# Kernel optimization log

Hardware: AMD Instinct MI355X
Metric: run time of the kernel (lower is better)

## Reference

```python
import jax, jax.numpy as jnp
import numpy as np

B_, L_, D_, E_, N_, DT_, K_ = 2, 1024, 1024, 2048, 16, 64, 4
EPS = 1e-5


def setup_inputs() -> dict:
    key = jax.random.key(0)
    ks = jax.random.split(key, 16)
    s = lambda *sh: 1.0 / np.sqrt(sh[-1])
    return {
        "resid": jax.random.normal(ks[0], (B_, L_, D_), jnp.float32),
        "norm_w": jnp.ones((D_,), jnp.float32),
        "skip_w": jax.random.normal(ks[1], (E_, D_), jnp.float32) * s(E_, D_),
        "in_w": jax.random.normal(ks[2], (E_, D_), jnp.float32) * s(E_, D_),
        "conv_w": jax.random.normal(ks[3], (E_, K_), jnp.float32) * s(E_, K_),
        "conv_b": jax.random.normal(ks[4], (E_,), jnp.float32) * 0.1,
        "wd1": jax.random.normal(ks[5], (DT_, E_), jnp.float32) * s(DT_, E_),
        "wd2": jax.random.normal(ks[6], (E_, DT_), jnp.float32) * s(E_, DT_),
        "wd2_b": jax.random.normal(ks[7], (E_,), jnp.float32) * 0.1,
        "wb": jax.random.normal(ks[8], (N_, E_), jnp.float32) * s(N_, E_),
        "wc": jax.random.normal(ks[9], (N_, E_), jnp.float32) * s(N_, E_),
        "A_log": jnp.log(jax.random.uniform(ks[10], (E_, N_), jnp.float32, 0.5, 4.0)),
        "W_D": jnp.ones((E_,), jnp.float32),
        "out_w": jax.random.normal(ks[11], (D_, E_), jnp.float32) * s(D_, E_),
    }


def _forward(resid, norm_w, skip_w, in_w, conv_w, conv_b, wd1, wd2, wd2_b,
             wb, wc, A_log, W_D, out_w):
    B, L, D = resid.shape
    E, N = A_log.shape
    K = conv_w.shape[-1]
    # RMSNorm
    xn = resid * jax.lax.rsqrt(jnp.mean(resid * resid, -1, keepdims=True) + EPS) * norm_w
    skip = jnp.einsum('bld,ed->ble', xn, skip_w)
    x = jnp.einsum('bld,ed->ble', xn, in_w)
    # causal depthwise conv1d (torch pads both sides by K-1, output cut to [:L])
    xp = jnp.pad(x, ((0, 0), (K - 1, 0), (0, 0)))
    conv = conv_b + sum(xp[:, k:k + L, :] * conv_w[:, k] for k in range(K))
    x = jax.nn.silu(conv)  # [B,L,E] ssm input
    # input-dependent projections
    delta = jax.nn.softplus(jnp.einsum('ble,re->blr', x, wd1) @ wd2.T + wd2_b)  # [B,L,E]
    Bt = jnp.einsum('ble,ne->bln', x, wb)  # [B,L,N]
    Ct = jnp.einsum('ble,ne->bln', x, wc)  # [B,L,N]
    A = -jnp.exp(A_log)  # [E,N]

    def step(h, inp):
        dt, b_t, c_t, x_t = inp  # [B,E],[B,N],[B,N],[B,E]
        A_bar = jnp.exp(dt[:, :, None] * A)          # [B,E,N]
        h = A_bar * h + (dt * x_t)[:, :, None] * b_t[:, None, :]
        y = jnp.einsum('ben,bn->be', h, c_t)
        return h, y

    h0 = jnp.zeros((B, E, N), x.dtype)
    xs = (delta.transpose(1, 0, 2), Bt.transpose(1, 0, 2),
          Ct.transpose(1, 0, 2), x.transpose(1, 0, 2))
    _, y = jax.lax.scan(step, h0, xs)
    y = y.transpose(1, 0, 2)  # [B,L,E]
    y = y + x * W_D
    y = y * jax.nn.silu(skip)
    y = jnp.einsum('ble,de->bld', y, out_w)
    return resid + y


def reference(resid, norm_w, skip_w, in_w, conv_w, conv_b, wd1, wd2, wd2_b,
              wb, wc, A_log, W_D, out_w):
    return _forward(resid, norm_w, skip_w, in_w, conv_w, conv_b, wd1, wd2,
                    wd2_b, wb, wc, A_log, W_D, out_w)
```

## Files before the change

kernel.cpp:

```cpp
#include <hip/hip_runtime.h>
#include <cstdint>

typedef unsigned short u16;
typedef float f32x4 __attribute__((ext_vector_type(4)));
typedef __bf16 bf16x8 __attribute__((ext_vector_type(8)));
typedef u16 u16x8 __attribute__((ext_vector_type(8)));

__device__ __forceinline__ u16 f2bf(float f) {
  uint32_t u = __float_as_uint(f);
  u += 0x7fffu + ((u >> 16) & 1u);
  return (u16)(u >> 16);
}
__device__ __forceinline__ float bf2f(u16 s) {
  return __uint_as_float(((uint32_t)s) << 16);
}

__device__ __forceinline__ void ld16(const u16* g, u16* l) {
  auto* gp = reinterpret_cast<const __attribute__((address_space(1))) u16*>(
      reinterpret_cast<uintptr_t>(g));
  auto* lp = reinterpret_cast<__attribute__((address_space(3))) u16*>(
      static_cast<uint32_t>(reinterpret_cast<uintptr_t>(l)));
  __builtin_amdgcn_global_load_lds(gp, lp, 16, 0, 0);
}

__device__ __forceinline__ f32x4 mfma16(u16x8 a, u16x8 b, f32x4 c) {
  return __builtin_amdgcn_mfma_f32_16x16x32_bf16(
      __builtin_bit_cast(bf16x8, a), __builtin_bit_cast(bf16x8, b), c, 0, 0, 0);
}

__device__ __forceinline__ float sigmoidf_(float x) { return 1.f / (1.f + __expf(-x)); }
__device__ __forceinline__ float siluf_(float x) { return x * sigmoidf_(x); }
__device__ __forceinline__ float softplusf_(float x) {
  return fmaxf(x, 0.f) + log1pf(__expf(-fabsf(x)));
}

#define PACK_TOT 6651904
__global__ __launch_bounds__(256) void pack_rms_kernel(
    const float* __restrict__ skip_w, const float* __restrict__ in_w,
    const float* __restrict__ out_w, const float* __restrict__ wd2,
    const float* __restrict__ wd1, const float* __restrict__ wb,
    const float* __restrict__ wc, const float* __restrict__ A_log,
    u16* __restrict__ skipw_bf, u16* __restrict__ inw_bf, u16* __restrict__ outw_bf,
    u16* __restrict__ wd2_bf, u16* __restrict__ w96, float* __restrict__ Aneg,
    const float* __restrict__ resid, const float* __restrict__ norm_w,
    u16* __restrict__ xn_bf) {
  int t = threadIdx.x;
  if (blockIdx.x >= 1024) {
    int row = blockIdx.x - 1024;
    const float4* xr = (const float4*)(resid + (size_t)row * 1024);
    float4 v = xr[t];
    float ss = v.x * v.x + v.y * v.y + v.z * v.z + v.w * v.w;
    for (int o = 32; o > 0; o >>= 1) ss += __shfl_xor(ss, o);
    __shared__ float wsum[4];
    if ((t & 63) == 0) wsum[t >> 6] = ss;
    __syncthreads();
    float tot = wsum[0] + wsum[1] + wsum[2] + wsum[3];
    float rs = rsqrtf(tot * (1.0f / 1024.0f) + 1e-5f);
    float4 wv = ((const float4*)norm_w)[t];
    uint2 pk;
    pk.x = (uint32_t)f2bf(v.x * rs * wv.x) | ((uint32_t)f2bf(v.y * rs * wv.y) << 16);
    pk.y = (uint32_t)f2bf(v.z * rs * wv.z) | ((uint32_t)f2bf(v.w * rs * wv.w) << 16);
    ((uint2*)xn_bf)[row * 256 + t] = pk;
    return;
  }
  const int stride = 1024 * 256;
  for (int i = blockIdx.x * 256 + t; i < PACK_TOT; i += stride) {
    int j = i;
    if (j < 2097152) { skipw_bf[j] = f2bf(skip_w[j]); continue; } j -= 2097152;
    if (j < 2097152) { inw_bf[j] = f2bf(in_w[j]); continue; } j -= 2097152;
    if (j < 2097152) { outw_bf[j] = f2bf(out_w[j]); continue; } j -= 2097152;
    if (j < 131072)  { wd2_bf[j] = f2bf(wd2[j]); continue; } j -= 131072;
    if (j < 131072)  { w96[j] = f2bf(wd1[j]); continue; } j -= 131072;
    if (j < 32768)   { w96[131072 + j] = f2bf(wb[j]); continue; } j -= 32768;
    if (j < 32768)   { w96[163840 + j] = f2bf(wc[j]); continue; } j -= 32768;
    Aneg[j] = -__expf(A_log[j]);
  }
}

template <int BM, int BN, int BK, int EPI>
__global__ __launch_bounds__(256) void gemm_bt(
    const u16* __restrict__ A, const u16* __restrict__ B0, const u16* __restrict__ B1,
    int M, int N, int K, int Nsplit,
    void* __restrict__ C0, void* __restrict__ C1,
    const float* __restrict__ bias, const float* __restrict__ addsrc) {
  constexpr int TM = BM / 32, TN = BN / 32;
  constexpr int KC = BK / 8;
  __shared__ __align__(16) u16 sA[BM * BK];
  __shared__ __align__(16) u16 sB[BN * BK];
  const int t = threadIdx.x;
  const int lane = t & 63, wid = t >> 6;
  const int wm = wid >> 1, wn = wid & 1;
  const int mBase = blockIdx.y * BM;
  const int nBase = blockIdx.x * BN;
  const bool hi = (nBase >= Nsplit);
  const u16* Bp = hi ? B1 : B0;
  const int nB0 = nBase - (hi ? Nsplit : 0);
  const int col = lane & 15, quad = lane >> 4;

  f32x4 acc[TM][TN];
#pragma unroll
  for (int i = 0; i < TM; ++i)
#pragma unroll
    for (int j = 0; j < TN; ++j) acc[i][j] = f32x4{0.f, 0.f, 0.f, 0.f};

  for (int k0 = 0; k0 < K; k0 += BK) {
#pragma unroll
    for (int c = t; c < BM * KC; c += 256) {
      int row = c / KC, j = c % KC;
      int k8 = ((j + row) & (KC - 1)) * 8;
      ld16(A + (size_t)(mBase + row) * K + k0 + k8, &sA[c * 8]);
    }
#pragma unroll
    for (int c = t; c < BN * KC; c += 256) {
      int row = c / KC, j = c % KC;
      int k8 = ((j + row) & (KC - 1)) * 8;
      ld16(Bp + (size_t)(nB0 + row) * K + k0 + k8, &sB[c * 8]);
    }
    __syncthreads();
#pragma unroll
    for (int kk = 0; kk < BK / 32; ++kk) {
      u16x8 af[TM], bfv[TN];
#pragma unroll
      for (int i = 0; i < TM; ++i) {
        int rowA = wm * (BM / 2) + i * 16 + col;
        af[i] = *(const u16x8*)&sA[rowA * BK + (((kk * 4 + quad) - rowA) & (KC - 1)) * 8];
      }
#pragma unroll
      for (int j = 0; j < TN; ++j) {
        int rowB = wn * (BN / 2) + j * 16 + col;
        bfv[j] = *(const u16x8*)&sB[rowB * BK + (((kk * 4 + quad) - rowB) & (KC - 1)) * 8];
      }
#pragma unroll
      for (int i = 0; i < TM; ++i)
#pragma unroll
        for (int j = 0; j < TN; ++j) acc[i][j] = mfma16(af[i], bfv[j], acc[i][j]);
    }
    __syncthreads();
  }

#pragma unroll
  for (int i = 0; i < TM; ++i) {
#pragma unroll
    for (int j = 0; j < TN; ++j) {
#pragma unroll
      for (int r = 0; r < 4; ++r) {
        int gm = mBase + wm * (BM / 2) + i * 16 + quad * 4 + r;
        int gn = nBase + wn * (BN / 2) + j * 16 + col;
        float v = acc[i][j][r];
        if (EPI == 0) {
          if (gn < Nsplit)
            ((u16*)C0)[(size_t)gm * Nsplit + gn] = f2bf(v);
          else
            ((u16*)C1)[(size_t)gm * (N - Nsplit) + (gn - Nsplit)] = f2bf(v);
        } else if (EPI == 1) {
          ((u16*)C0)[(size_t)gm * N + gn] = f2bf(softplusf_(v + bias[gn]));
        } else {
          ((float*)C0)[(size_t)gm * N + gn] = addsrc[(size_t)gm * N + gn] + v;
        }
      }
    }
  }
}

__global__ __launch_bounds__(256) void conv_skinny_kernel(
    const u16* __restrict__ xin_bf, const float* __restrict__ conv_w,
    const float* __restrict__ conv_b, u16* __restrict__ xconv_bf,
    const u16* __restrict__ w96, float* __restrict__ part) {
  constexpr int PAD = 264;
  __shared__ __align__(16) u16 sA[64 * PAD];
  __shared__ __align__(16) u16 sB[96 * 128];
  const int t = threadIdx.x, lane = t & 63, w = t >> 6;
  const int mBase = blockIdx.x * 64;
  const int e0 = blockIdx.y * 256;

  {
    const int ep = (t & 127) * 2;
    const int strip = t >> 7;
    const int ms = mBase + strip * 32;
    const int l0 = ms & 1023;
    const uint32_t* xr = (const uint32_t*)xin_bf;
    size_t base = ((size_t)ms * 2048 + e0 + ep) >> 1;
    int eg = e0 + ep;
    float4 w0 = ((const float4*)conv_w)[eg];
    float4 w1 = ((const float4*)conv_w)[eg + 1];
    float b0 = conv_b[eg], b1 = conv_b[eg + 1];
    uint32_t u;
    u = (l0 >= 1) ? xr[base - 1024] : 0u;
    float h10 = bf2f((u16)u), h11 = bf2f((u16)(u >> 16));
    u = (l0 >= 2) ? xr[base - 2048] : 0u;
    float h20 = bf2f((u16)u), h21 = bf2f((u16)(u >> 16));
    u = (l0 >= 3) ? xr[base - 3072] : 0u;
    float h30 = bf2f((u16)u), h31 = bf2f((u16)(u >> 16));
#pragma unroll 4
    for (int r = 0; r < 32; ++r) {
      uint32_t ux = xr[base + (size_t)r * 1024];
      float x0 = bf2f((u16)ux), x1 = bf2f((u16)(ux >> 16));
      float a0 = b0 + w0.w * x0 + w0.z * h10 + w0.y * h20 + w0.x * h30;
      float a1 = b1 + w1.w * x1 + w1.z * h11 + w1.y * h21 + w1.x * h31;
      a0 = siluf_(a0); a1 = siluf_(a1);
      uint32_t pk = (uint32_t)f2bf(a0) | ((uint32_t)f2bf(a1) << 16);
      ((uint32_t*)xconv_bf)[base + (size_t)r * 1024] = pk;
      *(uint32_t*)&sA[(strip * 32 + r) * PAD + ep] = pk;
      h30 = h20; h31 = h21; h20 = h10; h21 = h11; h10 = x0; h11 = x1;
    }
  }
  for (int c = t; c < 96 * 16; c += 256) {
    int row = c >> 4, j = c & 15;
    int k8 = ((j + row) & 15) * 8;
    ld16(w96 + (size_t)row * 2048 + e0 + k8, &sB[c * 8]);
  }
  __syncthreads();
  const int col = lane & 15, quad = lane >> 4;
  const int rowA = w * 16 + col;
  f32x4 acc[6];
#pragma unroll
  for (int j = 0; j < 6; ++j) acc[j] = f32x4{0.f, 0.f, 0.f, 0.f};
#pragma unroll
  for (int kk = 0; kk < 4; ++kk) {
    u16x8 af = *(const u16x8*)&sA[rowA * PAD + kk * 32 + quad * 8];
#pragma unroll
    for (int j = 0; j < 6; ++j) {
      int rowB = j * 16 + col;
      u16x8 bfv = *(const u16x8*)&sB[rowB * 128 + (((kk * 4 + quad) - rowB) & 15) * 8];
      acc[j] = mfma16(af, bfv, acc[j]);
    }
  }
  __syncthreads();
  for (int c = t; c < 96 * 16; c += 256) {
    int row = c >> 4, j = c & 15;
    int k8 = ((j + row) & 15) * 8;
    ld16(w96 + (size_t)row * 2048 + e0 + 128 + k8, &sB[c * 8]);
  }
  __syncthreads();
#pragma unroll
  for (int kk = 4; kk < 8; ++kk) {
    u16x8 af = *(const u16x8*)&sA[rowA * PAD + kk * 32 + quad * 8];
#pragma unroll
    for (int j = 0; j < 6; ++j) {
      int rowB = j * 16 + col;
      u16x8 bfv = *(const u16x8*)&sB[rowB * 128 + ((((kk - 4) * 4 + quad) - rowB) & 15) * 8];
      acc[j] = mfma16(af, bfv, acc[j]);
    }
  }
  float* pp = part + (size_t)blockIdx.y * (2048 * 96);
#pragma unroll
  for (int j = 0; j < 6; ++j)
#pragma unroll
    for (int r = 0; r < 4; ++r) {
      int gm = mBase + w * 16 + quad * 4 + r;
      int gn = j * 16 + col;
      pp[gm * 96 + gn] = acc[j][r];
    }
}

__global__ __launch_bounds__(256) void skinny_reduce(
    const float* __restrict__ part, u16* __restrict__ d1_bf,
    float* __restrict__ bc) {
  int i = blockIdx.x * 256 + threadIdx.x;
  float s = 0.f;
#pragma unroll
  for (int kc = 0; kc < 8; ++kc) s += part[kc * 196608 + i];
  int m = i / 96, n = i - m * 96;
  if (n < 64) d1_bf[m * 64 + n] = f2bf(s);
  else bc[m * 32 + n - 64] = s;
}

__global__ __launch_bounds__(256) void scan1_kernel(
    const u16* __restrict__ delta_bf, const u16* __restrict__ xconv_bf,
    const float* __restrict__ bc, const float* __restrict__ Aneg,
    float* __restrict__ hloc, float* __restrict__ Ssum) {
  int t = threadIdx.x;
  int e = blockIdx.x * 256 + t;
  int c = blockIdx.y, b = blockIdx.z;
  int m0 = b * 1024 + c * 32;
  __shared__ float sBC[1024];
  for (int j = t; j < 1024; j += 256) sBC[j] = bc[m0 * 32 + j];
  float Ar[16], h[16];
#pragma unroll
  for (int n = 0; n < 16; ++n) { Ar[n] = Aneg[e * 16 + n]; h[n] = 0.f; }
  float S = 0.f;
  __syncthreads();
  for (int l = 0; l < 32; ++l) {
    size_t m = (size_t)(m0 + l) * 2048 + e;
    float dt = bf2f(delta_bf[m]), xv = bf2f(xconv_bf[m]);
    S += dt;
    float dx = dt * xv;
    const float* bl = &sBC[l * 32];
#pragma unroll
    for (int n = 0; n < 16; ++n) h[n] = __expf(dt * Ar[n]) * h[n] + dx * bl[n];
  }
  size_t base = ((size_t)(b * 32 + c) * 2048 + e) * 16;
#pragma unroll
  for (int n = 0; n < 16; ++n) hloc[base + n] = h[n];
  Ssum[(b * 32 + c) * 2048 + e] = S;
}

__global__ __launch_bounds__(256) void combine_kernel(
    const float* __restrict__ Aneg, const float* __restrict__ Ssum,
    float* __restrict__ hloc) {
  int tid = blockIdx.x * 256 + threadIdx.x;
  int b = tid >> 15, r = tid & 32767;
  int e = r >> 4;
  float a = Aneg[r];
  float h = 0.f;
  for (int c = 0; c < 32; ++c) {
    size_t base = (size_t)(b * 32 + c) * 32768 + r;
    float hl = hloc[base];
    float S = Ssum[(b * 32 + c) * 2048 + e];
    hloc[base] = h;
    h = __expf(a * S) * h + hl;
  }
}

__global__ __launch_bounds__(256) void scan2_kernel(
    const u16* __restrict__ delta_bf, const u16* __restrict__ xconv_bf,
    const float* __restrict__ bc, const float* __restrict__ Aneg,
    const float* __restrict__ hloc, const u16* __restrict__ skip_bf,
    const float* __restrict__ W_D, u16* __restrict__ yfin_bf) {
  int t = threadIdx.x;
  int e = blockIdx.x * 256 + t;
  int c = blockIdx.y, b = blockIdx.z;
  int m0 = b * 1024 + c * 32;
  __shared__ float sBC[1024];
  for (int j = t; j < 1024; j += 256) sBC[j] = bc[m0 * 32 + j];
  float Ar[16], h[16];
  size_t hbase = ((size_t)(b * 32 + c) * 2048 + e) * 16;
#pragma unroll
  for (int n = 0; n < 16; ++n) { Ar[n] = Aneg[e * 16 + n]; h[n] = hloc[hbase + n]; }
  float wd = W_D[e];
  __syncthreads();
  for (int l = 0; l < 32; ++l) {
    size_t m = (size_t)(m0 + l) * 2048 + e;
    float dt = bf2f(delta_bf[m]), xv = bf2f(xconv_bf[m]);
    float dx = dt * xv;
    const float* bl = &sBC[l * 32];
    float y = 0.f;
#pragma unroll
    for (int n = 0; n < 16; ++n) {
      h[n] = __expf(dt * Ar[n]) * h[n] + dx * bl[n];
      y += h[n] * bl[16 + n];
    }
    float yv = y + xv * wd;
    float sk = bf2f(skip_bf[m]);
    yv *= sk * sigmoidf_(sk);
    yfin_bf[m] = f2bf(yv);
  }
}

extern "C" void kernel_launch(void* const* d_in, const int* in_sizes, int n_in,
                              void* d_out, int out_size, void* d_ws, size_t ws_size,
                              hipStream_t stream) {
  (void)in_sizes; (void)n_in; (void)out_size; (void)ws_size;
  const float* resid  = (const float*)d_in[0];
  const float* norm_w = (const float*)d_in[1];
  const float* skip_w = (const float*)d_in[2];
  const float* in_w   = (const float*)d_in[3];
  const float* conv_w = (const float*)d_in[4];
  const float* conv_b = (const float*)d_in[5];
  const float* wd1    = (const float*)d_in[6];
  const float* wd2    = (const float*)d_in[7];
  const float* wd2_b  = (const float*)d_in[8];
  const float* wb     = (const float*)d_in[9];
  const float* wc     = (const float*)d_in[10];
  const float* A_log  = (const float*)d_in[11];
  const float* W_D    = (const float*)d_in[12];
  const float* out_w  = (const float*)d_in[13];

  char* p = (char*)d_ws;
  u16*   skipw_bf = (u16*)(p + 0);
  u16*   inw_bf   = (u16*)(p + 4194304);
  u16*   outw_bf  = (u16*)(p + 8388608);
  u16*   wd2_bf   = (u16*)(p + 12582912);
  u16*   w96      = (u16*)(p + 12845056);
  float* Aneg     = (float*)(p + 13238272);
  u16*   xn_bf    = (u16*)(p + 13369344);
  u16*   skip_bf  = (u16*)(p + 17563648);
  u16*   xin_bf   = (u16*)(p + 25952256);
  u16*   xconv_bf = (u16*)(p + 34340864);
  u16*   delta_bf = (u16*)(p + 42729472);
  u16*   d1_bf    = (u16*)(p + 51118080);
  float* bc       = (float*)(p + 51380224);
  u16*   yfin_bf  = (u16*)(p + 51642368);
  float* part     = (float*)(p + 60030976);
  float* hloc     = (float*)(p + 66322432);
  float* Ssum     = (float*)(p + 74711040);

  pack_rms_kernel<<<3072, 256, 0, stream>>>(
      skip_w, in_w, out_w, wd2, wd1, wb, wc, A_log,
      skipw_bf, inw_bf, outw_bf, wd2_bf, w96, Aneg,
      resid, norm_w, xn_bf);
  gemm_bt<128, 128, 64, 0><<<dim3(32, 16), 256, 0, stream>>>(
      xn_bf, skipw_bf, inw_bf, 2048, 4096, 1024, 2048,
      (void*)skip_bf, (void*)xin_bf, nullptr, nullptr);
  conv_skinny_kernel<<<dim3(32, 8), 256, 0, stream>>>(
      xin_bf, conv_w, conv_b, xconv_bf, w96, part);
  skinny_reduce<<<768, 256, 0, stream>>>(part, d1_bf, bc);
  gemm_bt<128, 128, 64, 1><<<dim3(16, 16), 256, 0, stream>>>(
      d1_bf, wd2_bf, wd2_bf, 2048, 2048, 64, 2048,
      (void*)delta_bf, nullptr, wd2_b, nullptr);
  scan1_kernel<<<dim3(8, 32, 2), 256, 0, stream>>>(delta_bf, xconv_bf, bc, Aneg,
                                                   hloc, Ssum);
  combine_kernel<<<256, 256, 0, stream>>>(Aneg, Ssum, hloc);
  scan2_kernel<<<dim3(8, 32, 2), 256, 0, stream>>>(delta_bf, xconv_bf, bc, Aneg, hloc,
                                                   skip_bf, W_D, yfin_bf);
  gemm_bt<64, 64, 128, 2><<<dim3(16, 32), 256, 0, stream>>>(
      yfin_bf, outw_bf, outw_bf, 2048, 1024, 2048, 1024,
      (void*)d_out, nullptr, nullptr, resid);
}
```

Baseline: 232.5 us.

## Fuse all pipeline stages into one persistent kernel with grid barriers

```diff
diff --git a/kernel.cpp b/kernel.cpp
--- a/kernel.cpp
+++ b/kernel.cpp
@@ -5,6 +5,9 @@
 typedef float f32x4 __attribute__((ext_vector_type(4)));
 typedef __bf16 bf16x8 __attribute__((ext_vector_type(8)));
 typedef u16 u16x8 __attribute__((ext_vector_type(8)));
+
+#define NBLK 512
+#define PACK_TOT 6651904
 
 __device__ __forceinline__ u16 f2bf(float f) {
   uint32_t u = __float_as_uint(f);
@@ -34,64 +37,43 @@
   return fmaxf(x, 0.f) + log1pf(__expf(-fabsf(x)));
 }
 
-#define PACK_TOT 6651904
-__global__ __launch_bounds__(256) void pack_rms_kernel(
-    const float* __restrict__ skip_w, const float* __restrict__ in_w,
-    const float* __restrict__ out_w, const float* __restrict__ wd2,
-    const float* __restrict__ wd1, const float* __restrict__ wb,
-    const float* __restrict__ wc, const float* __restrict__ A_log,
-    u16* __restrict__ skipw_bf, u16* __restrict__ inw_bf, u16* __restrict__ outw_bf,
-    u16* __restrict__ wd2_bf, u16* __restrict__ w96, float* __restrict__ Aneg,
-    const float* __restrict__ resid, const float* __restrict__ norm_w,
-    u16* __restrict__ xn_bf) {
-  int t = threadIdx.x;
-  if (blockIdx.x >= 1024) {
-    int row = blockIdx.x - 1024;
-    const float4* xr = (const float4*)(resid + (size_t)row * 1024);
-    float4 v = xr[t];
-    float ss = v.x * v.x + v.y * v.y + v.z * v.z + v.w * v.w;
-    for (int o = 32; o > 0; o >>= 1) ss += __shfl_xor(ss, o);
-    __shared__ float wsum[4];
-    if ((t & 63) == 0) wsum[t >> 6] = ss;
-    __syncthreads();
-    float tot = wsum[0] + wsum[1] + wsum[2] + wsum[3];
-    float rs = rsqrtf(tot * (1.0f / 1024.0f) + 1e-5f);
-    float4 wv = ((const float4*)norm_w)[t];
-    uint2 pk;
-    pk.x = (uint32_t)f2bf(v.x * rs * wv.x) | ((uint32_t)f2bf(v.y * rs * wv.y) << 16);
-    pk.y = (uint32_t)f2bf(v.z * rs * wv.z) | ((uint32_t)f2bf(v.w * rs * wv.w) << 16);
-    ((uint2*)xn_bf)[row * 256 + t] = pk;
-    return;
-  }
-  const int stride = 1024 * 256;
-  for (int i = blockIdx.x * 256 + t; i < PACK_TOT; i += stride) {
-    int j = i;
-    if (j < 2097152) { skipw_bf[j] = f2bf(skip_w[j]); continue; } j -= 2097152;
-    if (j < 2097152) { inw_bf[j] = f2bf(in_w[j]); continue; } j -= 2097152;
-    if (j < 2097152) { outw_bf[j] = f2bf(out_w[j]); continue; } j -= 2097152;
-    if (j < 131072)  { wd2_bf[j] = f2bf(wd2[j]); continue; } j -= 131072;
-    if (j < 131072)  { w96[j] = f2bf(wd1[j]); continue; } j -= 131072;
-    if (j < 32768)   { w96[131072 + j] = f2bf(wb[j]); continue; } j -= 32768;
-    if (j < 32768)   { w96[163840 + j] = f2bf(wc[j]); continue; } j -= 32768;
-    Aneg[j] = -__expf(A_log[j]);
-  }
-}
+__device__ __forceinline__ void gsync(uint32_t* bar, int idx) {
+  __syncthreads();
+  if (threadIdx.x == 0) {
+    __threadfence();
+    __hip_atomic_fetch_add(&bar[idx], 1u, __ATOMIC_RELEASE, __HIP_MEMORY_SCOPE_AGENT);
+    while (__hip_atomic_load(&bar[idx], __ATOMIC_ACQUIRE,
+                             __HIP_MEMORY_SCOPE_AGENT) < (uint32_t)NBLK) {
+      __builtin_amdgcn_s_sleep(1);
+    }
+    __threadfence();
+  }
+  __syncthreads();
+}
+
+struct Args {
+  const float *resid, *norm_w, *skip_w, *in_w, *conv_w, *conv_b, *wd1, *wd2,
+      *wd2_b, *wb, *wc, *A_log, *W_D, *out_w;
+  u16 *skipw_bf, *inw_bf, *outw_bf, *wd2_bf, *w96, *xn_bf, *skip_bf, *xin_bf,
+      *xconv_bf, *delta_bf, *d1_bf, *yfin_bf;
+  float *Aneg, *bc, *part, *hloc, *Ssum, *out;
+  uint32_t* bar;
+};
 
 template <int BM, int BN, int BK, int EPI>
-__global__ __launch_bounds__(256) void gemm_bt(
-    const u16* __restrict__ A, const u16* __restrict__ B0, const u16* __restrict__ B1,
-    int M, int N, int K, int Nsplit,
+__device__ void gemm_phase(char* smem, int bx, int by,
+    const u16* __restrict__ A, const u16* __restrict__ B0,
+    const u16* __restrict__ B1, int N, int K, int Nsplit,
     void* __restrict__ C0, void* __restrict__ C1,
     const float* __restrict__ bias, const float* __restrict__ addsrc) {
-  constexpr int TM = BM / 32, TN = BN / 32;
-  constexpr int KC = BK / 8;
-  __shared__ __align__(16) u16 sA[BM * BK];
-  __shared__ __align__(16) u16 sB[BN * BK];
+  constexpr int TM = BM / 32, TN = BN / 32, KC = BK / 8;
+  u16* sA = (u16*)smem;
+  u16* sB = (u16*)smem + BM * BK;
   const int t = threadIdx.x;
   const int lane = t & 63, wid = t >> 6;
   const int wm = wid >> 1, wn = wid & 1;
-  const int mBase = blockIdx.y * BM;
-  const int nBase = blockIdx.x * BN;
+  const int mBase = by * BM;
+  const int nBase = bx * BN;
   const bool hi = (nBase >= Nsplit);
   const u16* Bp = hi ? B1 : B0;
   const int nB0 = nBase - (hi ? Nsplit : 0);
@@ -162,28 +144,25 @@
   }
 }
 
-__global__ __launch_bounds__(256) void conv_skinny_kernel(
-    const u16* __restrict__ xin_bf, const float* __restrict__ conv_w,
-    const float* __restrict__ conv_b, u16* __restrict__ xconv_bf,
-    const u16* __restrict__ w96, float* __restrict__ part) {
+__device__ void conv_skinny_phase(char* smem, int bxm, int byk, const Args& a) {
   constexpr int PAD = 264;
-  __shared__ __align__(16) u16 sA[64 * PAD];
-  __shared__ __align__(16) u16 sB[96 * 128];
+  u16* sA = (u16*)smem;
+  u16* sB = (u16*)(smem + 64 * PAD * 2);
   const int t = threadIdx.x, lane = t & 63, w = t >> 6;
-  const int mBase = blockIdx.x * 64;
-  const int e0 = blockIdx.y * 256;
+  const int mBase = bxm * 64;
+  const int e0 = byk * 256;
 
   {
     const int ep = (t & 127) * 2;
     const int strip = t >> 7;
     const int ms = mBase + strip * 32;
     const int l0 = ms & 1023;
-    const uint32_t* xr = (const uint32_t*)xin_bf;
+    const uint32_t* xr = (const uint32_t*)a.xin_bf;
     size_t base = ((size_t)ms * 2048 + e0 + ep) >> 1;
     int eg = e0 + ep;
-    float4 w0 = ((const float4*)conv_w)[eg];
-    float4 w1 = ((const float4*)conv_w)[eg + 1];
-    float b0 = conv_b[eg], b1 = conv_b[eg + 1];
+    float4 w0 = ((const float4*)a.conv_w)[eg];
+    float4 w1 = ((const float4*)a.conv_w)[eg + 1];
+    float b0 = a.conv_b[eg], b1 = a.conv_b[eg + 1];
     uint32_t u;
     u = (l0 >= 1) ? xr[base - 1024] : 0u;
     float h10 = bf2f((u16)u), h11 = bf2f((u16)(u >> 16));
@@ -199,7 +178,7 @@
       float a1 = b1 + w1.w * x1 + w1.z * h11 + w1.y * h21 + w1.x * h31;
       a0 = siluf_(a0); a1 = siluf_(a1);
       uint32_t pk = (uint32_t)f2bf(a0) | ((uint32_t)f2bf(a1) << 16);
-      ((uint32_t*)xconv_bf)[base + (size_t)r * 1024] = pk;
+      ((uint32_t*)a.xconv_bf)[base + (size_t)r * 1024] = pk;
       *(uint32_t*)&sA[(strip * 32 + r) * PAD + ep] = pk;
       h30 = h20; h31 = h21; h20 = h10; h21 = h11; h10 = x0; h11 = x1;
     }
@@ -207,7 +186,7 @@
   for (int c = t; c < 96 * 16; c += 256) {
     int row = c >> 4, j = c & 15;
     int k8 = ((j + row) & 15) * 8;
-    ld16(w96 + (size_t)row * 2048 + e0 + k8, &sB[c * 8]);
+    ld16(a.w96 + (size_t)row * 2048 + e0 + k8, &sB[c * 8]);
   }
   __syncthreads();
   const int col = lane & 15, quad = lane >> 4;
@@ -229,7 +208,7 @@
   for (int c = t; c < 96 * 16; c += 256) {
     int row = c >> 4, j = c & 15;
     int k8 = ((j + row) & 15) * 8;
-    ld16(w96 + (size_t)row * 2048 + e0 + 128 + k8, &sB[c * 8]);
+    ld16(a.w96 + (size_t)row * 2048 + e0 + 128 + k8, &sB[c * 8]);
   }
   __syncthreads();
 #pragma unroll
@@ -242,7 +221,7 @@
       acc[j] = mfma16(af, bfv, acc[j]);
     }
   }
-  float* pp = part + (size_t)blockIdx.y * (2048 * 96);
+  float* pp = a.part + (size_t)byk * (2048 * 96);
 #pragma unroll
   for (int j = 0; j < 6; ++j)
 #pragma unroll
@@ -253,97 +232,153 @@
     }
 }
 
-__global__ __launch_bounds__(256) void skinny_reduce(
-    const float* __restrict__ part, u16* __restrict__ d1_bf,
-    float* __restrict__ bc) {
-  int i = blockIdx.x * 256 + threadIdx.x;
-  float s = 0.f;
-#pragma unroll
-  for (int kc = 0; kc < 8; ++kc) s += part[kc * 196608 + i];
-  int m = i / 96, n = i - m * 96;
-  if (n < 64) d1_bf[m * 64 + n] = f2bf(s);
-  else bc[m * 32 + n - 64] = s;
-}
-
-__global__ __launch_bounds__(256) void scan1_kernel(
-    const u16* __restrict__ delta_bf, const u16* __restrict__ xconv_bf,
-    const float* __restrict__ bc, const float* __restrict__ Aneg,
-    float* __restrict__ hloc, float* __restrict__ Ssum) {
-  int t = threadIdx.x;
-  int e = blockIdx.x * 256 + t;
-  int c = blockIdx.y, b = blockIdx.z;
-  int m0 = b * 1024 + c * 32;
-  __shared__ float sBC[1024];
-  for (int j = t; j < 1024; j += 256) sBC[j] = bc[m0 * 32 + j];
-  float Ar[16], h[16];
-#pragma unroll
-  for (int n = 0; n < 16; ++n) { Ar[n] = Aneg[e * 16 + n]; h[n] = 0.f; }
-  float S = 0.f;
-  __syncthreads();
-  for (int l = 0; l < 32; ++l) {
-    size_t m = (size_t)(m0 + l) * 2048 + e;
-    float dt = bf2f(delta_bf[m]), xv = bf2f(xconv_bf[m]);
-    S += dt;
-    float dx = dt * xv;
-    const float* bl = &sBC[l * 32];
-#pragma unroll
-    for (int n = 0; n < 16; ++n) h[n] = __expf(dt * Ar[n]) * h[n] + dx * bl[n];
-  }
-  size_t base = ((size_t)(b * 32 + c) * 2048 + e) * 16;
-#pragma unroll
-  for (int n = 0; n < 16; ++n) hloc[base + n] = h[n];
-  Ssum[(b * 32 + c) * 2048 + e] = S;
-}
-
-__global__ __launch_bounds__(256) void combine_kernel(
-    const float* __restrict__ Aneg, const float* __restrict__ Ssum,
-    float* __restrict__ hloc) {
-  int tid = blockIdx.x * 256 + threadIdx.x;
-  int b = tid >> 15, r = tid & 32767;
-  int e = r >> 4;
-  float a = Aneg[r];
-  float h = 0.f;
-  for (int c = 0; c < 32; ++c) {
-    size_t base = (size_t)(b * 32 + c) * 32768 + r;
-    float hl = hloc[base];
-    float S = Ssum[(b * 32 + c) * 2048 + e];
-    hloc[base] = h;
-    h = __expf(a * S) * h + hl;
-  }
-}
-
-__global__ __launch_bounds__(256) void scan2_kernel(
-    const u16* __restrict__ delta_bf, const u16* __restrict__ xconv_bf,
-    const float* __restrict__ bc, const float* __restrict__ Aneg,
-    const float* __restrict__ hloc, const u16* __restrict__ skip_bf,
-    const float* __restrict__ W_D, u16* __restrict__ yfin_bf) {
-  int t = threadIdx.x;
-  int e = blockIdx.x * 256 + t;
-  int c = blockIdx.y, b = blockIdx.z;
-  int m0 = b * 1024 + c * 32;
-  __shared__ float sBC[1024];
-  for (int j = t; j < 1024; j += 256) sBC[j] = bc[m0 * 32 + j];
-  float Ar[16], h[16];
-  size_t hbase = ((size_t)(b * 32 + c) * 2048 + e) * 16;
-#pragma unroll
-  for (int n = 0; n < 16; ++n) { Ar[n] = Aneg[e * 16 + n]; h[n] = hloc[hbase + n]; }
-  float wd = W_D[e];
-  __syncthreads();
-  for (int l = 0; l < 32; ++l) {
-    size_t m = (size_t)(m0 + l) * 2048 + e;
-    float dt = bf2f(delta_bf[m]), xv = bf2f(xconv_bf[m]);
-    float dx = dt * xv;
-    const float* bl = &sBC[l * 32];
-    float y = 0.f;
-#pragma unroll
-    for (int n = 0; n < 16; ++n) {
-      h[n] = __expf(dt * Ar[n]) * h[n] + dx * bl[n];
-      y += h[n] * bl[16 + n];
-    }
-    float yv = y + xv * wd;
-    float sk = bf2f(skip_bf[m]);
-    yv *= sk * sigmoidf_(sk);
-    yfin_bf[m] = f2bf(yv);
+__global__ __launch_bounds__(256, 2) void mega_kernel(Args a) {
+  __shared__ __align__(16) char smem[58368];
+  const int bid = blockIdx.x;
+  const int t = threadIdx.x;
+
+  for (int v = bid; v < 3072; v += NBLK) {
+    if (v >= 1024) {
+      int row = v - 1024;
+      const float4* xr = (const float4*)(a.resid + (size_t)row * 1024);
+      float4 vv = xr[t];
+      float ss = vv.x * vv.x + vv.y * vv.y + vv.z * vv.z + vv.w * vv.w;
+      for (int o = 32; o > 0; o >>= 1) ss += __shfl_xor(ss, o);
+      float* wsum = (float*)smem;
+      if ((t & 63) == 0) wsum[t >> 6] = ss;
+      __syncthreads();
+      float tot = wsum[0] + wsum[1] + wsum[2] + wsum[3];
+      float rs = rsqrtf(tot * (1.0f / 1024.0f) + 1e-5f);
+      float4 wv = ((const float4*)a.norm_w)[t];
+      uint2 pk;
+      pk.x = (uint32_t)f2bf(vv.x * rs * wv.x) | ((uint32_t)f2bf(vv.y * rs * wv.y) << 16);
+      pk.y = (uint32_t)f2bf(vv.z * rs * wv.z) | ((uint32_t)f2bf(vv.w * rs * wv.w) << 16);
+      ((uint2*)a.xn_bf)[row * 256 + t] = pk;
+      __syncthreads();
+    } else {
+      for (int i = v * 256 + t; i < PACK_TOT; i += 1024 * 256) {
+        int j = i;
+        if (j < 2097152) { a.skipw_bf[j] = f2bf(a.skip_w[j]); continue; } j -= 2097152;
+        if (j < 2097152) { a.inw_bf[j] = f2bf(a.in_w[j]); continue; } j -= 2097152;
+        if (j < 2097152) { a.outw_bf[j] = f2bf(a.out_w[j]); continue; } j -= 2097152;
+        if (j < 131072)  { a.wd2_bf[j] = f2bf(a.wd2[j]); continue; } j -= 131072;
+        if (j < 131072)  { a.w96[j] = f2bf(a.wd1[j]); continue; } j -= 131072;
+        if (j < 32768)   { a.w96[131072 + j] = f2bf(a.wb[j]); continue; } j -= 32768;
+        if (j < 32768)   { a.w96[163840 + j] = f2bf(a.wc[j]); continue; } j -= 32768;
+        a.Aneg[j] = -__expf(a.A_log[j]);
+      }
+    }
+  }
+  gsync(a.bar, 0);
+
+  {
+    int xcd = bid & 7, slot = bid >> 3;
+    int bx = xcd * 4 + (slot & 3), by = slot >> 2;
+    gemm_phase<128, 128, 64, 0>(smem, bx, by, a.xn_bf, a.skipw_bf, a.inw_bf,
+                                4096, 1024, 2048, a.skip_bf, a.xin_bf,
+                                nullptr, nullptr);
+  }
+  gsync(a.bar, 1);
+
+  if (bid < 256) conv_skinny_phase(smem, bid & 31, bid >> 5, a);
+  gsync(a.bar, 2);
+
+  for (int i = bid * 256 + t; i < 196608; i += NBLK * 256) {
+    float s = 0.f;
+#pragma unroll
+    for (int kc = 0; kc < 8; ++kc) s += a.part[kc * 196608 + i];
+    int m = i / 96, n = i - m * 96;
+    if (n < 64) a.d1_bf[m * 64 + n] = f2bf(s);
+    else a.bc[m * 32 + n - 64] = s;
+  }
+  gsync(a.bar, 3);
+
+  if (bid < 256)
+    gemm_phase<128, 128, 64, 1>(smem, bid & 15, bid >> 4, a.d1_bf, a.wd2_bf,
+                                a.wd2_bf, 2048, 64, 2048, a.delta_bf, nullptr,
+                                a.wd2_b, nullptr);
+  gsync(a.bar, 4);
+
+  {
+    int eb = bid & 7, c = (bid >> 3) & 31, b = bid >> 8;
+    int e = eb * 256 + t;
+    int m0 = b * 1024 + c * 32;
+    float* sBC = (float*)smem;
+    for (int j = t; j < 1024; j += 256) sBC[j] = a.bc[m0 * 32 + j];
+    float Ar[16], h[16];
+#pragma unroll
+    for (int n = 0; n < 16; ++n) { Ar[n] = a.Aneg[e * 16 + n]; h[n] = 0.f; }
+    float S = 0.f;
+    __syncthreads();
+    for (int l = 0; l < 32; ++l) {
+      size_t m = (size_t)(m0 + l) * 2048 + e;
+      float dt = bf2f(a.delta_bf[m]), xv = bf2f(a.xconv_bf[m]);
+      S += dt;
+      float dx = dt * xv;
+      const float* bl = &sBC[l * 32];
+#pragma unroll
+      for (int n = 0; n < 16; ++n) h[n] = __expf(dt * Ar[n]) * h[n] + dx * bl[n];
+    }
+    size_t base = ((size_t)(b * 32 + c) * 2048 + e) * 16;
+#pragma unroll
+    for (int n = 0; n < 16; ++n) a.hloc[base + n] = h[n];
+    a.Ssum[(b * 32 + c) * 2048 + e] = S;
+  }
+  gsync(a.bar, 5);
+
+  if (bid < 256) {
+    int tid = bid * 256 + t;
+    int b = tid >> 15, r = tid & 32767;
+    int e = r >> 4;
+    float av = a.Aneg[r];
+    float h = 0.f;
+    for (int c = 0; c < 32; ++c) {
+      size_t base = (size_t)(b * 32 + c) * 32768 + r;
+      float hl = a.hloc[base];
+      float S = a.Ssum[(b * 32 + c) * 2048 + e];
+      a.hloc[base] = h;
+      h = __expf(av * S) * h + hl;
+    }
+  }
+  gsync(a.bar, 6);
+
+  {
+    int eb = bid & 7, c = (bid >> 3) & 31, b = bid >> 8;
+    int e = eb * 256 + t;
+    int m0 = b * 1024 + c * 32;
+    float* sBC = (float*)smem;
+    for (int j = t; j < 1024; j += 256) sBC[j] = a.bc[m0 * 32 + j];
+    float Ar[16], h[16];
+    size_t hbase = ((size_t)(b * 32 + c) * 2048 + e) * 16;
+#pragma unroll
+    for (int n = 0; n < 16; ++n) { Ar[n] = a.Aneg[e * 16 + n]; h[n] = a.hloc[hbase + n]; }
+    float wd = a.W_D[e];
+    __syncthreads();
+    for (int l = 0; l < 32; ++l) {
+      size_t m = (size_t)(m0 + l) * 2048 + e;
+      float dt = bf2f(a.delta_bf[m]), xv = bf2f(a.xconv_bf[m]);
+      float dx = dt * xv;
+      const float* bl = &sBC[l * 32];
+      float y = 0.f;
+#pragma unroll
+      for (int n = 0; n < 16; ++n) {
+        h[n] = __expf(dt * Ar[n]) * h[n] + dx * bl[n];
+        y += h[n] * bl[16 + n];
+      }
+      float yv = y + xv * wd;
+      float sk = bf2f(a.skip_bf[m]);
+      yv *= sk * sigmoidf_(sk);
+      a.yfin_bf[m] = f2bf(yv);
+    }
+  }
+  gsync(a.bar, 7);
+
+  if (bid < 256) {
+    int xcd = bid & 7, slot = bid >> 3;
+    int bx = xcd * 2 + (slot & 1), by = slot >> 1;
+    gemm_phase<128, 64, 64, 2>(smem, bx, by, a.yfin_bf, a.outw_bf, a.outw_bf,
+                               1024, 2048, 1024, a.out, nullptr, nullptr,
+                               a.resid);
   }
 }
 
@@ -351,59 +386,43 @@
                               void* d_out, int out_size, void* d_ws, size_t ws_size,
                               hipStream_t stream) {
   (void)in_sizes; (void)n_in; (void)out_size; (void)ws_size;
-  const float* resid  = (const float*)d_in[0];
-  const float* norm_w = (const float*)d_in[1];
-  const float* skip_w = (const float*)d_in[2];
-  const float* in_w   = (const float*)d_in[3];
-  const float* conv_w = (const float*)d_in[4];
-  const float* conv_b = (const float*)d_in[5];
-  const float* wd1    = (const float*)d_in[6];
-  const float* wd2    = (const float*)d_in[7];
-  const float* wd2_b  = (const float*)d_in[8];
-  const float* wb     = (const float*)d_in[9];
-  const float* wc     = (const float*)d_in[10];
-  const float* A_log  = (const float*)d_in[11];
-  const float* W_D    = (const float*)d_in[12];
-  const float* out_w  = (const float*)d_in[13];
-
   char* p = (char*)d_ws;
-  u16*   skipw_bf = (u16*)(p + 0);
-  u16*   inw_bf   = (u16*)(p + 4194304);
-  u16*   outw_bf  = (u16*)(p + 8388608);
-  u16*   wd2_bf   = (u16*)(p + 12582912);
-  u16*   w96      = (u16*)(p + 12845056);
-  float* Aneg     = (float*)(p + 13238272);
-  u16*   xn_bf    = (u16*)(p + 13369344);
-  u16*   skip_bf  = (u16*)(p + 17563648);
-  u16*   xin_bf   = (u16*)(p + 25952256);
-  u16*   xconv_bf = (u16*)(p + 34340864);
-  u16*   delta_bf = (u16*)(p + 42729472);
-  u16*   d1_bf    = (u16*)(p + 51118080);
-  float* bc       = (float*)(p + 51380224);
-  u16*   yfin_bf  = (u16*)(p + 51642368);
-  float* part     = (float*)(p + 60030976);
-  float* hloc     = (float*)(p + 66322432);
-  float* Ssum     = (float*)(p + 74711040);
-
-  pack_rms_kernel<<<3072, 256, 0, stream>>>(
-      skip_w, in_w, out_w, wd2, wd1, wb, wc, A_log,
-      skipw_bf, inw_bf, outw_bf, wd2_bf, w96, Aneg,
-      resid, norm_w, xn_bf);
-  gemm_bt<128, 128, 64, 0><<<dim3(32, 16), 256, 0, stream>>>(
-      xn_bf, skipw_bf, inw_bf, 2048, 4096, 1024, 2048,
-      (void*)skip_bf, (void*)xin_bf, nullptr, nullptr);
-  conv_skinny_kernel<<<dim3(32, 8), 256, 0, stream>>>(
-      xin_bf, conv_w, conv_b, xconv_bf, w96, part);
-  skinny_reduce<<<768, 256, 0, stream>>>(part, d1_bf, bc);
-  gemm_bt<128, 128, 64, 1><<<dim3(16, 16), 256, 0, stream>>>(
-      d1_bf, wd2_bf, wd2_bf, 2048, 2048, 64, 2048,
-      (void*)delta_bf, nullptr, wd2_b, nullptr);
-  scan1_kernel<<<dim3(8, 32, 2), 256, 0, stream>>>(delta_bf, xconv_bf, bc, Aneg,
-                                                   hloc, Ssum);
-  combine_kernel<<<256, 256, 0, stream>>>(Aneg, Ssum, hloc);
-  scan2_kernel<<<dim3(8, 32, 2), 256, 0, stream>>>(delta_bf, xconv_bf, bc, Aneg, hloc,
-                                                   skip_bf, W_D, yfin_bf);
-  gemm_bt<64, 64, 128, 2><<<dim3(16, 32), 256, 0, stream>>>(
-      yfin_bf, outw_bf, outw_bf, 2048, 1024, 2048, 1024,
-      (void*)d_out, nullptr, nullptr, resid);
-}
+  Args a;
+  a.resid  = (const float*)d_in[0];
+  a.norm_w = (const float*)d_in[1];
+  a.skip_w = (const float*)d_in[2];
+  a.in_w   = (const float*)d_in[3];
+  a.conv_w = (const float*)d_in[4];
+  a.conv_b = (const float*)d_in[5];
+  a.wd1    = (const float*)d_in[6];
+  a.wd2    = (const float*)d_in[7];
+  a.wd2_b  = (const float*)d_in[8];
+  a.wb     = (const float*)d_in[9];
+  a.wc     = (const float*)d_in[10];
+  a.A_log  = (const float*)d_in[11];
+  a.W_D    = (const float*)d_in[12];
+  a.out_w  = (const float*)d_in[13];
+
+  a.skipw_bf = (u16*)(p + 0);
+  a.inw_bf   = (u16*)(p + 4194304);
+  a.outw_bf  = (u16*)(p + 8388608);
+  a.wd2_bf   = (u16*)(p + 12582912);
+  a.w96      = (u16*)(p + 12845056);
+  a.Aneg     = (float*)(p + 13238272);
+  a.xn_bf    = (u16*)(p + 13369344);
+  a.skip_bf  = (u16*)(p + 17563648);
+  a.xin_bf   = (u16*)(p + 25952256);
+  a.xconv_bf = (u16*)(p + 34340864);
+  a.delta_bf = (u16*)(p + 42729472);
+  a.d1_bf    = (u16*)(p + 51118080);
+  a.bc       = (float*)(p + 51380224);
+  a.yfin_bf  = (u16*)(p + 51642368);
+  a.part     = (float*)(p + 60030976);
+  a.hloc     = (float*)(p + 66322432);
+  a.Ssum     = (float*)(p + 74711040);
+  a.bar      = (uint32_t*)(p + 104857600);
+  a.out      = (float*)d_out;
+
+  hipMemsetAsync((void*)a.bar, 0, 64 * sizeof(uint32_t), stream);
+  mega_kernel<<<NBLK, 256, 0, stream>>>(a);
+}
```

After: 914.8 us. +293.4%, slower.

## Fuse delta projection into scan kernels and atomically reduce skinny split-K

Applied to the files above, without the earlier changes.

```diff
diff --git a/kernel.cpp b/kernel.cpp
--- a/kernel.cpp
+++ b/kernel.cpp
@@ -82,7 +82,7 @@
     const u16* __restrict__ A, const u16* __restrict__ B0, const u16* __restrict__ B1,
     int M, int N, int K, int Nsplit,
     void* __restrict__ C0, void* __restrict__ C1,
-    const float* __restrict__ bias, const float* __restrict__ addsrc) {
+    const float* __restrict__ addsrc) {
   constexpr int TM = BM / 32, TN = BN / 32;
   constexpr int KC = BK / 8;
   __shared__ __align__(16) u16 sA[BM * BK];
@@ -152,8 +152,6 @@
             ((u16*)C0)[(size_t)gm * Nsplit + gn] = f2bf(v);
           else
             ((u16*)C1)[(size_t)gm * (N - Nsplit) + (gn - Nsplit)] = f2bf(v);
-        } else if (EPI == 1) {
-          ((u16*)C0)[(size_t)gm * N + gn] = f2bf(softplusf_(v + bias[gn]));
         } else {
           ((float*)C0)[(size_t)gm * N + gn] = addsrc[(size_t)gm * N + gn] + v;
         }
@@ -165,7 +163,7 @@
 __global__ __launch_bounds__(256) void conv_skinny_kernel(
     const u16* __restrict__ xin_bf, const float* __restrict__ conv_w,
     const float* __restrict__ conv_b, u16* __restrict__ xconv_bf,
-    const u16* __restrict__ w96, float* __restrict__ part) {
+    const u16* __restrict__ w96, float* __restrict__ dbc) {
   constexpr int PAD = 264;
   __shared__ __align__(16) u16 sA[64 * PAD];
   __shared__ __align__(16) u16 sB[96 * 128];
@@ -242,47 +240,70 @@
       acc[j] = mfma16(af, bfv, acc[j]);
     }
   }
-  float* pp = part + (size_t)blockIdx.y * (2048 * 96);
 #pragma unroll
   for (int j = 0; j < 6; ++j)
 #pragma unroll
     for (int r = 0; r < 4; ++r) {
       int gm = mBase + w * 16 + quad * 4 + r;
       int gn = j * 16 + col;
-      pp[gm * 96 + gn] = acc[j][r];
-    }
-}
-
-__global__ __launch_bounds__(256) void skinny_reduce(
-    const float* __restrict__ part, u16* __restrict__ d1_bf,
-    float* __restrict__ bc) {
-  int i = blockIdx.x * 256 + threadIdx.x;
-  float s = 0.f;
-#pragma unroll
-  for (int kc = 0; kc < 8; ++kc) s += part[kc * 196608 + i];
-  int m = i / 96, n = i - m * 96;
-  if (n < 64) d1_bf[m * 64 + n] = f2bf(s);
-  else bc[m * 32 + n - 64] = s;
+      atomicAdd(&dbc[gm * 96 + gn], acc[j][r]);
+    }
+}
+
+__device__ __forceinline__ void delta_tile(
+    const float* __restrict__ dbc, const u16* __restrict__ wd2_bf,
+    const float* __restrict__ wd2_b, int m0, int e0,
+    u16* sD1, float* sDT, float* sBC) {
+  const int t = threadIdx.x;
+  for (int i = t; i < 2048; i += 256)
+    sD1[i] = f2bf(dbc[(m0 + (i >> 6)) * 96 + (i & 63)]);
+  for (int j = t; j < 1024; j += 256)
+    sBC[j] = dbc[(m0 + (j >> 5)) * 96 + 64 + (j & 31)];
+  __syncthreads();
+  const int lane = t & 63, wid = t >> 6;
+  const int col = lane & 15, quad = lane >> 4;
+  const int mt = wid & 1, ntB = (wid >> 1) * 8;
+  u16x8 afr0 = *(const u16x8*)&sD1[(mt * 16 + col) * 64 + quad * 8];
+  u16x8 afr1 = *(const u16x8*)&sD1[(mt * 16 + col) * 64 + 32 + quad * 8];
+#pragma unroll
+  for (int jj = 0; jj < 8; ++jj) {
+    int ecol = (ntB + jj) * 16 + col;
+    int erow = e0 + ecol;
+    u16x8 b0 = *(const u16x8*)&wd2_bf[(size_t)erow * 64 + quad * 8];
+    u16x8 b1 = *(const u16x8*)&wd2_bf[(size_t)erow * 64 + 32 + quad * 8];
+    f32x4 dacc = f32x4{0.f, 0.f, 0.f, 0.f};
+    dacc = mfma16(afr0, b0, dacc);
+    dacc = mfma16(afr1, b1, dacc);
+    float bias = wd2_b[erow];
+#pragma unroll
+    for (int r = 0; r < 4; ++r)
+      sDT[(mt * 16 + quad * 4 + r) * 260 + ecol] = softplusf_(dacc[r] + bias);
+  }
+  __syncthreads();
 }
 
 __global__ __launch_bounds__(256) void scan1_kernel(
-    const u16* __restrict__ delta_bf, const u16* __restrict__ xconv_bf,
-    const float* __restrict__ bc, const float* __restrict__ Aneg,
-    float* __restrict__ hloc, float* __restrict__ Ssum) {
-  int t = threadIdx.x;
-  int e = blockIdx.x * 256 + t;
-  int c = blockIdx.y, b = blockIdx.z;
-  int m0 = b * 1024 + c * 32;
+    const float* __restrict__ dbc, const u16* __restrict__ wd2_bf,
+    const float* __restrict__ wd2_b, const u16* __restrict__ xconv_bf,
+    const float* __restrict__ Aneg, float* __restrict__ hloc,
+    float* __restrict__ Ssum) {
+  __shared__ __align__(16) float sDT[32 * 260];
+  __shared__ __align__(16) u16 sD1[32 * 64];
   __shared__ float sBC[1024];
-  for (int j = t; j < 1024; j += 256) sBC[j] = bc[m0 * 32 + j];
+  const int t = threadIdx.x;
+  const int eb = blockIdx.x, c = blockIdx.y, b = blockIdx.z;
+  const int e0 = eb * 256;
+  const int m0 = b * 1024 + c * 32;
+  delta_tile(dbc, wd2_bf, wd2_b, m0, e0, sD1, sDT, sBC);
+  const int e = e0 + t;
   float Ar[16], h[16];
 #pragma unroll
   for (int n = 0; n < 16; ++n) { Ar[n] = Aneg[e * 16 + n]; h[n] = 0.f; }
   float S = 0.f;
-  __syncthreads();
   for (int l = 0; l < 32; ++l) {
     size_t m = (size_t)(m0 + l) * 2048 + e;
-    float dt = bf2f(delta_bf[m]), xv = bf2f(xconv_bf[m]);
+    float dt = sDT[l * 260 + t];
+    float xv = bf2f(xconv_bf[m]);
     S += dt;
     float dx = dt * xv;
     const float* bl = &sBC[l * 32];
@@ -313,25 +334,29 @@
 }
 
 __global__ __launch_bounds__(256) void scan2_kernel(
-    const u16* __restrict__ delta_bf, const u16* __restrict__ xconv_bf,
-    const float* __restrict__ bc, const float* __restrict__ Aneg,
-    const float* __restrict__ hloc, const u16* __restrict__ skip_bf,
-    const float* __restrict__ W_D, u16* __restrict__ yfin_bf) {
-  int t = threadIdx.x;
-  int e = blockIdx.x * 256 + t;
-  int c = blockIdx.y, b = blockIdx.z;
-  int m0 = b * 1024 + c * 32;
+    const float* __restrict__ dbc, const u16* __restrict__ wd2_bf,
+    const float* __restrict__ wd2_b, const u16* __restrict__ xconv_bf,
+    const float* __restrict__ Aneg, const float* __restrict__ hloc,
+    const u16* __restrict__ skip_bf, const float* __restrict__ W_D,
+    u16* __restrict__ yfin_bf) {
+  __shared__ __align__(16) float sDT[32 * 260];
+  __shared__ __align__(16) u16 sD1[32 * 64];
   __shared__ float sBC[1024];
-  for (int j = t; j < 1024; j += 256) sBC[j] = bc[m0 * 32 + j];
+  const int t = threadIdx.x;
+  const int eb = blockIdx.x, c = blockIdx.y, b = blockIdx.z;
+  const int e0 = eb * 256;
+  const int m0 = b * 1024 + c * 32;
+  delta_tile(dbc, wd2_bf, wd2_b, m0, e0, sD1, sDT, sBC);
+  const int e = e0 + t;
   float Ar[16], h[16];
   size_t hbase = ((size_t)(b * 32 + c) * 2048 + e) * 16;
 #pragma unroll
   for (int n = 0; n < 16; ++n) { Ar[n] = Aneg[e * 16 + n]; h[n] = hloc[hbase + n]; }
   float wd = W_D[e];
-  __syncthreads();
   for (int l = 0; l < 32; ++l) {
     size_t m = (size_t)(m0 + l) * 2048 + e;
-    float dt = bf2f(delta_bf[m]), xv = bf2f(xconv_bf[m]);
+    float dt = sDT[l * 260 + t];
+    float xv = bf2f(xconv_bf[m]);
     float dx = dt * xv;
     const float* bl = &sBC[l * 32];
     float y = 0.f;
@@ -377,33 +402,27 @@
   u16*   skip_bf  = (u16*)(p + 17563648);
   u16*   xin_bf   = (u16*)(p + 25952256);
   u16*   xconv_bf = (u16*)(p + 34340864);
-  u16*   delta_bf = (u16*)(p + 42729472);
-  u16*   d1_bf    = (u16*)(p + 51118080);
-  float* bc       = (float*)(p + 51380224);
-  u16*   yfin_bf  = (u16*)(p + 51642368);
-  float* part     = (float*)(p + 60030976);
-  float* hloc     = (float*)(p + 66322432);
-  float* Ssum     = (float*)(p + 74711040);
-
+  float* dbc      = (float*)(p + 42729472);
+  u16*   yfin_bf  = (u16*)(p + 43515904);
+  float* hloc     = (float*)(p + 51904512);
+  float* Ssum     = (float*)(p + 60293120);
+
+  hipMemsetAsync((void*)dbc, 0, 2048 * 96 * sizeof(float), stream);
   pack_rms_kernel<<<3072, 256, 0, stream>>>(
       skip_w, in_w, out_w, wd2, wd1, wb, wc, A_log,
       skipw_bf, inw_bf, outw_bf, wd2_bf, w96, Aneg,
       resid, norm_w, xn_bf);
   gemm_bt<128, 128, 64, 0><<<dim3(32, 16), 256, 0, stream>>>(
       xn_bf, skipw_bf, inw_bf, 2048, 4096, 1024, 2048,
-      (void*)skip_bf, (void*)xin_bf, nullptr, nullptr);
+      (void*)skip_bf, (void*)xin_bf, nullptr);
   conv_skinny_kernel<<<dim3(32, 8), 256, 0, stream>>>(
-      xin_bf, conv_w, conv_b, xconv_bf, w96, part);
-  skinny_reduce<<<768, 256, 0, stream>>>(part, d1_bf, bc);
-  gemm_bt<128, 128, 64, 1><<<dim3(16, 16), 256, 0, stream>>>(
-      d1_bf, wd2_bf, wd2_bf, 2048, 2048, 64, 2048,
-      (void*)delta_bf, nullptr, wd2_b, nullptr);
-  scan1_kernel<<<dim3(8, 32, 2), 256, 0, stream>>>(delta_bf, xconv_bf, bc, Aneg,
-                                                   hloc, Ssum);
+      xin_bf, conv_w, conv_b, xconv_bf, w96, dbc);
+  scan1_kernel<<<dim3(8, 32, 2), 256, 0, stream>>>(
+      dbc, wd2_bf, wd2_b, xconv_bf, Aneg, hloc, Ssum);
   combine_kernel<<<256, 256, 0, stream>>>(Aneg, Ssum, hloc);
-  scan2_kernel<<<dim3(8, 32, 2), 256, 0, stream>>>(delta_bf, xconv_bf, bc, Aneg, hloc,
-                                                   skip_bf, W_D, yfin_bf);
+  scan2_kernel<<<dim3(8, 32, 2), 256, 0, stream>>>(
+      dbc, wd2_bf, wd2_b, xconv_bf, Aneg, hloc, skip_bf, W_D, yfin_bf);
   gemm_bt<64, 64, 128, 2><<<dim3(16, 32), 256, 0, stream>>>(
       yfin_bf, outw_bf, outw_bf, 2048, 1024, 2048, 1024,
-      (void*)d_out, nullptr, nullptr, resid);
-}
+      (void*)d_out, nullptr, resid);
+}
```

After: 236.3 us. No clear change (+1.6%).
